# Performance work log

Measured on AMD Instinct MI355X. Metric: run time of the kernel, lower is better.

The kernel has to match this reference:

```python
import jax, jax.numpy as jnp
import numpy as np
import math

PAD_IDX = 1
BOS_IDX = 2
B, S, T = 32, 128, 64
E, H, L, V = 256, 512, 2, 32000


def _lstm_cell(gates, c):
    # torch gate order: i, f, g, o
    i, f, g, o = jnp.split(gates, 4, axis=-1)
    c_new = jax.nn.sigmoid(f) * c + jax.nn.sigmoid(i) * jnp.tanh(g)
    h_new = jax.nn.sigmoid(o) * jnp.tanh(c_new)
    return h_new, c_new


def _run_lstm_layer(x_tbi, Wih, Whh, b, h0, c0):
    def step(carry, x_t):
        h, c = carry
        h2, c2 = _lstm_cell(x_t @ Wih + h @ Whh + b, c)
        return (h2, c2), h2
    (hT, cT), ys = jax.lax.scan(step, (h0, c0), x_tbi)
    return ys, hT, cT


def setup_inputs() -> dict:
    key = jax.random.key(0)
    ks = iter(jax.random.split(key, 40))
    def w(shape, s=0.05):
        return jax.random.normal(next(ks), shape, jnp.float32) * s
    inp = {
        'src_tokens': jax.random.randint(next(ks), (B, S), 0, V, dtype=jnp.int32),
        'tgt_tokens': jax.random.randint(next(ks), (B, T), 0, V, dtype=jnp.int32),
        'src_emb': w((V, E), 0.02),
        'tgt_emb': w((V, E), 0.02),
        'enc_Wih0': w((E, 4 * H)), 'enc_Whh0': w((H, 4 * H)), 'enc_b0': jnp.zeros((4 * H,), jnp.float32),
        'enc_Wih1': w((H, 4 * H)), 'enc_Whh1': w((H, 4 * H)), 'enc_b1': jnp.zeros((4 * H,), jnp.float32),
        'dec_Wih0': w((E + H, 4 * H)), 'dec_Whh0': w((H, 4 * H)), 'dec_b0': jnp.zeros((4 * H,), jnp.float32),
        'dec_Wih1': w((H, 4 * H)), 'dec_Whh1': w((H, 4 * H)), 'dec_b1': jnp.zeros((4 * H,), jnp.float32),
        'attn_W': w((2 * H, H)), 'attn_b': jnp.zeros((H,), jnp.float32),
        'v_w': w((H,)),
        'coal_w': w((L, 1), 0.5), 'coal_b': jnp.zeros((1,), jnp.float32),
        'out_W': w((2 * H + E, V)), 'out_b': jnp.zeros((V,), jnp.float32),
    }
    return inp


def reference(src_tokens, tgt_tokens, src_emb, tgt_emb,
              enc_Wih0, enc_Whh0, enc_b0, enc_Wih1, enc_Whh1, enc_b1,
              dec_Wih0, dec_Whh0, dec_b0, dec_Wih1, dec_Whh1, dec_b1,
              attn_W, attn_b, v_w, coal_w, coal_b, out_W, out_b):
    Bq = src_tokens.shape[0]
    sqrtE_src = np.float32(math.sqrt(src_emb.shape[1]))
    sqrtE_tgt = np.float32(math.sqrt(tgt_emb.shape[1]))

    # ---- Encoder (2-layer LSTM, batch_first; dropout=0 eval) ----
    x = (src_emb[src_tokens] * sqrtE_src).transpose(1, 0, 2)  # (S,B,E)
    z = jnp.zeros((Bq, H), jnp.float32)
    ys0, hA, cA = _run_lstm_layer(x, enc_Wih0, enc_Whh0, enc_b0, z, z)
    ys1, hB, cB = _run_lstm_layer(ys0, enc_Wih1, enc_Whh1, enc_b1, z, z)
    enc_out = ys1.transpose(1, 0, 2)          # (B,S,H)
    hidden = jnp.stack([hA, hB])              # (L,B,H)
    cell = jnp.stack([cA, cB])

    mask = src_tokens != PAD_IDX              # (B,S)
    Wq, We = attn_W[:H], attn_W[H:]
    enc_proj = enc_out @ We                   # (B,S,H) loop-invariant part of attn linear

    def dec_step(carry, tok):
        h, c = carry                          # (L,B,H) each
        emb = jax.nn.relu(tgt_emb[tok] * sqrtE_tgt)          # (B,E)
        # faithful raw reshape (L,B,H) -> (B,H,L), coalesce layers
        q = jax.nn.relu(h.reshape(Bq, H, L) @ coal_w + coal_b)[..., 0]  # (B,H)
        e = jnp.tanh(enc_proj + (q @ Wq + attn_b)[:, None, :])          # (B,S,H)
        score = e @ v_w                                                 # (B,S)
        score = jnp.where(mask, score, np.float32(-1e10))
        a = jax.nn.softmax(score, axis=1)
        wctx = jnp.einsum('bs,bsh->bh', a, enc_out)                     # (B,H)
        xin = jnp.concatenate([emb, wctx], axis=-1)                     # (B,E+H)
        h0n, c0n = _lstm_cell(xin @ dec_Wih0 + h[0] @ dec_Whh0 + dec_b0, c[0])
        h1n, c1n = _lstm_cell(h0n @ dec_Wih1 + h[1] @ dec_Whh1 + dec_b1, c[1])
        logits = jnp.concatenate([h1n, wctx, emb], axis=-1) @ out_W + out_b  # (B,V)
        return (jnp.stack([h0n, h1n]), jnp.stack([c0n, c1n])), logits

    (hF, cF), outs = jax.lax.scan(dec_step, (hidden, cell), tgt_tokens[:, :-1].T)
    first = jnp.full((Bq, 1, out_b.shape[0]), np.float32(BOS_IDX))  # decoder_outputs[:,0]=BOS_IDX
    dec_outputs = jnp.concatenate([first, outs.transpose(1, 0, 2)], axis=1)  # (B,T,V)
    return dec_outputs, hF, cF
```

## Files before the change

kernel.cpp:

```cpp
#include <hip/hip_runtime.h>
#include <hip/hip_bf16.h>

typedef __bf16 bf16x8 __attribute__((ext_vector_type(8)));
typedef float f32x4 __attribute__((ext_vector_type(4)));
typedef unsigned long long u64;

#define DEV static __device__ __forceinline__

constexpr int Bq = 32, Sq = 128, Tq = 64, Eq = 256, Hq = 512, Vq = 32000;
constexpr int G4 = 2048;
constexpr int TD = 63;
constexpr int KOUT = 1280;
constexpr float SQRTE = 16.0f;

DEV float sigf(float x) { return 1.0f / (1.0f + __expf(-x)); }
DEV float tanh_fast(float x) {
    float ax = fabsf(x);
    float t = __expf(-2.f * ax);
    float r = (1.f - t) / (1.f + t);
    return x < 0.f ? -r : r;
}
DEV float tanh_c(float x) {
    float xc = fminf(fmaxf(x, -15.f), 15.f);
    float t = __expf(2.f * xc);
    return (t - 1.f) / (t + 1.f);
}

DEV u64 ldc(const u64* p) {
    return __hip_atomic_load(p, __ATOMIC_RELAXED, __HIP_MEMORY_SCOPE_AGENT);
}
DEV unsigned ldc32(const unsigned* p) {
    return __hip_atomic_load(p, __ATOMIC_RELAXED, __HIP_MEMORY_SCOPE_AGENT);
}
DEV void stc(u64* p, u64 v) {
    __hip_atomic_store(p, v, __ATOMIC_RELAXED, __HIP_MEMORY_SCOPE_AGENT);
}
DEV void stc32(unsigned* p, unsigned v) {
    __hip_atomic_store(p, v, __ATOMIC_RELAXED, __HIP_MEMORY_SCOPE_AGENT);
}
DEV unsigned short bfbits(float f) {
    __bf16 h = (__bf16)f;
    return __builtin_bit_cast(unsigned short, h);
}
DEV float bf2f(unsigned short u) {
    __bf16 h = __builtin_bit_cast(__bf16, u);
    return (float)h;
}
DEV u64 pack4bf(float a, float b, float c, float d) {
    return (u64)bfbits(a) | ((u64)bfbits(b) << 16) |
           ((u64)bfbits(c) << 32) | ((u64)bfbits(d) << 48);
}
DEV u64 pack2f(float a, float b) {
    return (u64)__float_as_uint(a) | ((u64)__float_as_uint(b) << 32);
}

DEV void gbar(unsigned* flags, int nblk, unsigned epoch) {
    __syncthreads();
    if (threadIdx.x < 64) {
        if (threadIdx.x == 0) {
            asm volatile("s_waitcnt vmcnt(0)" ::: "memory");
            stc32(flags + blockIdx.x * 32, epoch);
        }
        int lane = threadIdx.x;
        for (;;) {
            unsigned v0 = (lane < nblk) ? ldc32(flags + lane * 32) : epoch;
            unsigned v1 = (lane + 64 < nblk) ? ldc32(flags + (lane + 64) * 32) : epoch;
            if (__all((int)((v0 >= epoch) && (v1 >= epoch)))) break;
            __builtin_amdgcn_s_sleep(1);
        }
    }
    __syncthreads();
}

__global__ __launch_bounds__(256) void k_embed_src(const int* __restrict__ tok,
                                                   const float* __restrict__ emb,
                                                   __hip_bfloat16* __restrict__ x)
{
    int idx = blockIdx.x * 256 + threadIdx.x;
    int e = idx & (Eq - 1);
    int r = idx >> 8;
    int b = r & 31, t = r >> 5;
    x[idx] = __float2bfloat16(emb[(size_t)tok[b * Sq + t] * Eq + e] * SQRTE);
}

__global__ __launch_bounds__(256) void k_embed_tgt(const int* __restrict__ tok,
                                                   const float* __restrict__ emb,
                                                   __hip_bfloat16* __restrict__ embt,
                                                   __hip_bfloat16* __restrict__ Xout)
{
    int idx = blockIdx.x * 256 + threadIdx.x;
    int e = idx & (Eq - 1);
    int r = idx >> 8;
    int b = r & 31, t = r >> 5;
    float v = fmaxf(0.f, emb[(size_t)tok[b * Tq + t] * Eq + e] * SQRTE);
    embt[idx] = __float2bfloat16(v);
    Xout[(size_t)r * KOUT + 1024 + e] = __float2bfloat16(v);
}

__global__ __launch_bounds__(256) void k_transpose_bf16(const float* __restrict__ W,
                                                        __hip_bfloat16* __restrict__ Wt,
                                                        int K, int N)
{
    __shared__ float tile[32][33];
    int nb = blockIdx.x * 32, kb = blockIdx.y * 32;
    int c = threadIdx.x & 31, r4 = threadIdx.x >> 5;
    for (int i = 0; i < 32; i += 8)
        tile[r4 + i][c] = W[(size_t)(kb + r4 + i) * N + nb + c];
    __syncthreads();
    for (int i = 0; i < 32; i += 8) {
        int rr = r4 + i;
        Wt[(size_t)(nb + rr) * K + kb + c] = __float2bfloat16(tile[c][rr]);
    }
}

DEV void stage_coh(const u64* src, __bf16* As) {
    int tx = threadIdx.x;
#pragma unroll
    for (int p = 0; p < 8; ++p) {
        int c = tx + p * 256;
        int row = c >> 6, kc = c & 63;
        u64 v0 = ldc(src + c * 2);
        u64 v1 = ldc(src + c * 2 + 1);
        int kd = kc ^ (row & 7);
        *(u64*)(As + row * 512 + kd * 8) = v0;
        *(u64*)(As + row * 512 + kd * 8 + 4) = v1;
    }
}

DEV void mfma_pass(const __bf16* As, const unsigned short* BT, int colB,
                   int kg, int fr, f32x4* acc) {
    const unsigned short* bp = BT + (size_t)colB * 512 + kg * 8;
    int f7 = fr & 7;
#pragma unroll
    for (int k0 = 0; k0 < 512; k0 += 32) {
        int cidx = ((k0 >> 3) | kg) ^ f7;
        bf16x8 bfv = *(const bf16x8*)(bp + k0);
        bf16x8 af0 = *(const bf16x8*)(As + fr * 512 + cidx * 8);
        bf16x8 af1 = *(const bf16x8*)(As + (16 + fr) * 512 + cidx * 8);
        acc[0] = __builtin_amdgcn_mfma_f32_16x16x32_bf16(af0, bfv, acc[0], 0, 0, 0);
        acc[1] = __builtin_amdgcn_mfma_f32_16x16x32_bf16(af1, bfv, acc[1], 0, 0, 0);
    }
}

DEV void mfma_gates(const __bf16* As0, const __bf16* As1,
                    const __hip_bfloat16* B0T, const __hip_bfloat16* B1T,
                    int j0, float* gbuf)
{
    int tx = threadIdx.x, w = tx >> 6, lane = tx & 63;
    int fr = lane & 15, kg = lane >> 4;
    int colB = w * 512 + j0 + fr;
    f32x4 acc[2];
    acc[0] = (f32x4){0.f, 0.f, 0.f, 0.f};
    acc[1] = (f32x4){0.f, 0.f, 0.f, 0.f};
    mfma_pass(As0, (const unsigned short*)B0T, colB, kg, fr, acc);
    if (B1T) mfma_pass(As1, (const unsigned short*)B1T, colB, kg, fr, acc);
    __syncthreads();
    float* gw = gbuf + w * 512;
#pragma unroll
    for (int m = 0; m < 2; ++m)
#pragma unroll
        for (int qd = 0; qd < 4; ++qd)
            gw[(m * 16 + kg * 4 + qd) * 16 + fr] = acc[m][qd];
    __syncthreads();
}

DEV void gh_pass(const u64* hsrc, const __hip_bfloat16* WT,
                 float* slab_tile, int j0, __bf16* As0)
{
    stage_coh(hsrc, As0);
    __syncthreads();
    int tx = threadIdx.x, w = tx >> 6, lane = tx & 63;
    int fr = lane & 15, kg = lane >> 4;
    int colB = w * 512 + j0 + fr;
    f32x4 acc[2];
    acc[0] = (f32x4){0.f, 0.f, 0.f, 0.f};
    acc[1] = (f32x4){0.f, 0.f, 0.f, 0.f};
    mfma_pass(As0, (const unsigned short*)WT, colB, kg, fr, acc);
    float* outp = slab_tile + w * 512;
#pragma unroll
    for (int m = 0; m < 2; ++m)
#pragma unroll
        for (int qd = 0; qd < 4; ++qd)
            stc32((unsigned*)(outp + (m * 16 + kg * 4 + qd) * 16 + fr),
                  __float_as_uint(acc[m][qd]));
}

DEV void cell_epi(const float* gbuf, const float* gadd,
                  const __hip_bfloat16* xpart, const float* bias,
                  float* cbuf, u64* hb, u64* hf,
                  __hip_bfloat16* eb, int ebs, int j0)
{
    int tx = threadIdx.x;
    if (tx >= 128) return;
    int b = tx >> 2, jg = tx & 3;
    int jj0 = jg * 4;
    int j = j0 + jj0;
    float g[4][4];
#pragma unroll
    for (int gi = 0; gi < 4; ++gi) {
        int idx = gi * 512 + b * 16 + jj0;
        float4 gv = *(const float4*)(gbuf + idx);
        g[gi][0] = gv.x; g[gi][1] = gv.y; g[gi][2] = gv.z; g[gi][3] = gv.w;
        if (gadd) {
            u64 p0 = ldc((const u64*)gadd + (idx >> 1));
            u64 p1 = ldc((const u64*)gadd + (idx >> 1) + 1);
            g[gi][0] += __uint_as_float((unsigned)(p0 & 0xffffffffu));
            g[gi][1] += __uint_as_float((unsigned)(p0 >> 32));
            g[gi][2] += __uint_as_float((unsigned)(p1 & 0xffffffffu));
            g[gi][3] += __uint_as_float((unsigned)(p1 >> 32));
        }
        if (xpart) {
            u64 xv = *(const u64*)((const unsigned short*)xpart + b * 2048 + gi * 512 + j);
#pragma unroll
            for (int e = 0; e < 4; ++e)
                g[gi][e] += bf2f((unsigned short)(xv >> (16 * e)));
        }
        if (bias) {
            float4 bv = *(const float4*)(bias + gi * 512 + j);
            g[gi][0] += bv.x; g[gi][1] += bv.y; g[gi][2] += bv.z; g[gi][3] += bv.w;
        }
    }
    float4 cv = *(float4*)(cbuf + b * 512 + j);
    float cc[4] = {cv.x, cv.y, cv.z, cv.w};
    float hv[4];
#pragma unroll
    for (int e = 0; e < 4; ++e) {
        float cn = sigf(g[1][e]) * cc[e] + sigf(g[0][e]) * tanh_fast(g[2][e]);
        cc[e] = cn;
        hv[e] = sigf(g[3][e]) * tanh_fast(cn);
    }
    *(float4*)(cbuf + b * 512 + j) = make_float4(cc[0], cc[1], cc[2], cc[3]);
    u64 hpk = pack4bf(hv[0], hv[1], hv[2], hv[3]);
    stc(hb + ((b * 512 + j) >> 2), hpk);
    stc(hf + ((b * 512 + j) >> 1), pack2f(hv[0], hv[1]));
    stc(hf + ((b * 512 + j) >> 1) + 1, pack2f(hv[2], hv[3]));
    if (eb) *(u64*)(eb + (size_t)b * ebs + j) = hpk;
}

__global__ __launch_bounds__(256) void k_enc_persist(
    const __hip_bfloat16* __restrict__ X0b,
    const __hip_bfloat16* __restrict__ eWhh0T, const __hip_bfloat16* __restrict__ eWih1T,
    const __hip_bfloat16* __restrict__ eWhh1T, const float* __restrict__ eb1,
    __hip_bfloat16* __restrict__ h0b, __hip_bfloat16* __restrict__ h1b,
    float* __restrict__ h0f, float* __restrict__ h1f,
    float* __restrict__ c0, float* __restrict__ c1,
    __hip_bfloat16* __restrict__ ys0b,
    __hip_bfloat16* __restrict__ encb,
    unsigned* __restrict__ flags)
{
    __shared__ __align__(16) char shm[65536];
    __bf16* As0 = (__bf16*)shm;
    __bf16* As1 = (__bf16*)(shm + 32768);
    bool lay1 = blockIdx.x >= 32;
    int j0 = (blockIdx.x & 31) * 16;
    for (int t = 0; t <= 128; ++t) {
        if (!lay1) {
            if (t < 128) {
                stage_coh((const u64*)(h0b + (t & 1) * 16384), As0);
                __syncthreads();
                mfma_gates(As0, nullptr, eWhh0T, nullptr, j0, (float*)As0);
                cell_epi((float*)As0, nullptr, X0b + (size_t)t * 32 * 2048, nullptr,
                         c0, (u64*)(h0b + ((t + 1) & 1) * 16384), (u64*)h0f,
                         nullptr, 0, j0);
                if (threadIdx.x < 128) {
                    int b = threadIdx.x >> 2, jg = threadIdx.x & 3;
                    int j = j0 + jg * 4;
                    u64 hpk = ldc((const u64*)(h0b + ((t + 1) & 1) * 16384) + ((b * 512 + j) >> 2));
                    stc((u64*)(ys0b + (size_t)t * 16384 + b * 512 + j), hpk);
                }
            }
        } else {
            if (t >= 1) {
                int s = t - 1;
                stage_coh((const u64*)(ys0b + (size_t)s * 16384), As0);
                stage_coh((const u64*)(h1b + (s & 1) * 16384), As1);
                __syncthreads();
                mfma_gates(As0, As1, eWih1T, eWhh1T, j0, (float*)As0);
                cell_epi((float*)As0, nullptr, nullptr, eb1,
                         c1, (u64*)(h1b + ((s + 1) & 1) * 16384), (u64*)h1f,
                         encb + s * 512, 128 * 512, j0);
            }
        }
        gbar(flags, 64, (unsigned)(t + 1));
    }
}

__global__ __launch_bounds__(256) void k_dec_persist(
    const __hip_bfloat16* __restrict__ enc_projb, const __hip_bfloat16* __restrict__ enc_outb,
    const int* __restrict__ src_tok, const float* __restrict__ v_w,
    const float* __restrict__ attn_W, const float* __restrict__ attn_b,
    const float* __restrict__ coal_w, const float* __restrict__ coal_b,
    const __hip_bfloat16* __restrict__ dWih0wT, const __hip_bfloat16* __restrict__ dWhh0T,
    const __hip_bfloat16* __restrict__ dWih1T, const __hip_bfloat16* __restrict__ dWhh1T,
    const float* __restrict__ db1, const __hip_bfloat16* __restrict__ Xembb,
    float* __restrict__ h0fd, float* __restrict__ h1fd,
    __hip_bfloat16* __restrict__ h0bd, __hip_bfloat16* __restrict__ h1bd,
    float* __restrict__ c0d, float* __restrict__ c1d,
    __hip_bfloat16* __restrict__ wctxb,
    __hip_bfloat16* __restrict__ Xout,
    float* __restrict__ g0slab, float* __restrict__ g1slab,
    unsigned* __restrict__ flags)
{
    __shared__ __align__(16) char shm[32768];
    __shared__ float rinvs;
    __bf16* As0 = (__bf16*)shm;
    int bid = blockIdx.x, tx = threadIdx.x;
    unsigned bep = 0;

    for (int t = 0; t < TD; ++t) {
        int cur = t & 1, nxt = cur ^ 1;
        __hip_bfloat16* XoutT = Xout + (size_t)t * 32 * KOUT;

        if (bid < 32) {
            int b = bid;
            float* q   = (float*)shm;
            float* aqs = q + 512;
            float* vws = aqs + 512;
            float* ws  = vws + 512;
            const float* hrow = (b < 16) ? (h0fd + cur * 16384 + b * 1024)
                                         : (h1fd + cur * 16384 + (b - 16) * 1024);
            float cw0 = coal_w[0], cw1 = coal_w[1], cb = coal_b[0];
            for (int j = tx; j < 512; j += 256) {
                u64 pv = ldc((const u64*)hrow + j);
                float v0 = __uint_as_float((unsigned)(pv & 0xffffffffu));
                float v1 = __uint_as_float((unsigned)(pv >> 32));
                q[j] = fmaxf(0.f, v0 * cw0 + v1 * cw1 + cb);
            }
            for (int i = tx; i < 512; i += 256) vws[i] = v_w[i];
            __syncthreads();
            float a0 = attn_b[tx], a1 = attn_b[tx + 256];
#pragma unroll 8
            for (int j = 0; j < 512; ++j) {
                float qj = q[j];
                a0 += qj * attn_W[(size_t)j * 512 + tx];
                a1 += qj * attn_W[(size_t)j * 512 + tx + 256];
            }
            aqs[tx] = a0; aqs[tx + 256] = a1;
            __syncthreads();
            int s = tx >> 1, half = tx & 1;
            const unsigned short* epr = (const unsigned short*)enc_projb
                                        + ((size_t)(b * 128 + s)) * 512 + half * 256;
            float s0 = 0.f, s1 = 0.f, s2 = 0.f, s3 = 0.f;
#pragma unroll 4
            for (int ii = 0; ii < 256; ii += 8) {
                bf16x8 f8 = *(const bf16x8*)(epr + ii);
                int ib = half * 256 + ii;
                s0 += tanh_c((float)f8[0] + aqs[ib])     * vws[ib];
                s1 += tanh_c((float)f8[1] + aqs[ib + 1]) * vws[ib + 1];
                s2 += tanh_c((float)f8[2] + aqs[ib + 2]) * vws[ib + 2];
                s3 += tanh_c((float)f8[3] + aqs[ib + 3]) * vws[ib + 3];
                s0 += tanh_c((float)f8[4] + aqs[ib + 4]) * vws[ib + 4];
                s1 += tanh_c((float)f8[5] + aqs[ib + 5]) * vws[ib + 5];
                s2 += tanh_c((float)f8[6] + aqs[ib + 6]) * vws[ib + 6];
                s3 += tanh_c((float)f8[7] + aqs[ib + 7]) * vws[ib + 7];
            }
            float p = (s0 + s1) + (s2 + s3);
            p += __shfl_xor(p, 1, 64);
            if (half == 0)
                ws[s] = (src_tok[b * 128 + s] != 1) ? __expf(p) : 0.f;
            __syncthreads();
            if (tx < 64) {
                float ss = ws[tx] + ws[tx + 64];
#pragma unroll
                for (int o = 32; o > 0; o >>= 1) ss += __shfl_down(ss, o, 64);
                if (tx == 0) rinvs = 1.0f / ss;
            }
            __syncthreads();
            float rinv = rinvs;
            const unsigned short* eo = (const unsigned short*)enc_outb + (size_t)b * 65536;
            int i0 = tx * 2;
            float c0a = 0.f, c1a = 0.f;
#pragma unroll 4
            for (int s2i = 0; s2i < 128; ++s2i) {
                unsigned pk2 = *(const unsigned*)(eo + (size_t)s2i * 512 + i0);
                float wv = ws[s2i];
                c0a += wv * bf2f((unsigned short)(pk2 & 0xffffu));
                c1a += wv * bf2f((unsigned short)(pk2 >> 16));
            }
            c0a *= rinv; c1a *= rinv;
            unsigned pk = (unsigned)bfbits(c0a) | ((unsigned)bfbits(c1a) << 16);
            stc32((unsigned*)wctxb + ((b * 512 + i0) >> 1), pk);
            *((unsigned*)XoutT + (((size_t)b * KOUT + 512 + i0) >> 1)) = pk;
        } else if (bid < 64) {
            int tile = bid - 32;
            gh_pass((const u64*)(h0bd + cur * 16384), dWhh0T,
                    g0slab + tile * 2048, tile * 16, As0);
        } else {
            int tile = bid - 64;
            gh_pass((const u64*)(h1bd + cur * 16384), dWhh1T,
                    g1slab + tile * 2048, tile * 16, As0);
        }
        gbar(flags, 96, ++bep);

        if (bid < 32) {
            int j0 = bid * 16;
            stage_coh((const u64*)wctxb, As0);
            __syncthreads();
            mfma_gates(As0, nullptr, dWih0wT, nullptr, j0, (float*)As0);
            cell_epi((float*)As0, g0slab + bid * 2048,
                     Xembb + (size_t)t * 32 * 2048, nullptr,
                     c0d, (u64*)(h0bd + nxt * 16384), (u64*)(h0fd + nxt * 16384),
                     nullptr, 0, j0);
        }
        gbar(flags, 96, ++bep);

        if (bid < 32) {
            int j0 = bid * 16;
            stage_coh((const u64*)(h0bd + nxt * 16384), As0);
            __syncthreads();
            mfma_gates(As0, nullptr, dWih1T, nullptr, j0, (float*)As0);
            cell_epi((float*)As0, g1slab + bid * 2048,
                     nullptr, db1,
                     c1d, (u64*)(h1bd + nxt * 16384), (u64*)(h1fd + nxt * 16384),
                     XoutT, KOUT, j0);
        }
        gbar(flags, 96, ++bep);
    }
}

__global__ __launch_bounds__(256) void k_mfma(
    const __hip_bfloat16* __restrict__ A, const __hip_bfloat16* __restrict__ BT,
    const float* __restrict__ bias, float* __restrict__ Cf,
    __hip_bfloat16* __restrict__ Cb, int M, int N, int K)
{
    __shared__ __bf16 As[128][72];
    __shared__ __bf16 Bs[128][72];
    const unsigned short* Aw = (const unsigned short*)A;
    const unsigned short* Bw = (const unsigned short*)BT;
    int n0 = blockIdx.x * 128, m0 = blockIdx.y * 128;
    int tx = threadIdx.x;
    int w = tx >> 6, lane = tx & 63;
    int wm = (w >> 1) * 64, wn = (w & 1) * 64;
    int fr = lane & 15, kg = lane >> 4;
    f32x4 acc[4][4];
#pragma unroll
    for (int mi = 0; mi < 4; mi++)
#pragma unroll
        for (int ni = 0; ni < 4; ni++) acc[mi][ni] = (f32x4){0.f, 0.f, 0.f, 0.f};

    for (int k0 = 0; k0 < K; k0 += 64) {
        __syncthreads();
#pragma unroll
        for (int p = 0; p < 4; p++) {
            int ch = tx + p * 256;
            int r = ch >> 3, cc = (ch & 7) * 8;
            uint4 va = {0u, 0u, 0u, 0u};
            int m = m0 + r;
            if (m < M) va = *(const uint4*)(Aw + (size_t)m * K + k0 + cc);
            *(uint4*)(&As[r][cc]) = va;
            uint4 vb = *(const uint4*)(Bw + (size_t)(n0 + r) * K + k0 + cc);
            *(uint4*)(&Bs[r][cc]) = vb;
        }
        __syncthreads();
#pragma unroll
        for (int kk = 0; kk < 64; kk += 32) {
            bf16x8 af[4], bfv[4];
#pragma unroll
            for (int i = 0; i < 4; i++) {
                af[i]  = *(const bf16x8*)(&As[wm + i * 16 + fr][kk + kg * 8]);
                bfv[i] = *(const bf16x8*)(&Bs[wn + i * 16 + fr][kk + kg * 8]);
            }
#pragma unroll
            for (int mi = 0; mi < 4; mi++)
#pragma unroll
                for (int ni = 0; ni < 4; ni++)
                    acc[mi][ni] = __builtin_amdgcn_mfma_f32_16x16x32_bf16(
                        af[mi], bfv[ni], acc[mi][ni], 0, 0, 0);
        }
    }
#pragma unroll
    for (int ni = 0; ni < 4; ni++) {
        int n = n0 + wn + ni * 16 + fr;
        float bv = bias ? bias[n] : 0.f;
#pragma unroll
        for (int mi = 0; mi < 4; mi++) {
#pragma unroll
            for (int qd = 0; qd < 4; qd++) {
                int R = m0 + wm + mi * 16 + kg * 4 + qd;
                if (R < M) {
                    float v = acc[mi][ni][qd] + bv;
                    if (Cf) Cf[(size_t)R * N + n] = v;
                    else    Cb[(size_t)R * N + n] = __float2bfloat16(v);
                }
            }
        }
    }
}

__global__ __launch_bounds__(256) void k_init_dec(
    const float* __restrict__ h0e, const float* __restrict__ h1e,
    const float* __restrict__ c0e, const float* __restrict__ c1e,
    float* __restrict__ h0fd, float* __restrict__ h1fd,
    __hip_bfloat16* __restrict__ h0bd, __hip_bfloat16* __restrict__ h1bd,
    float* __restrict__ c0d, float* __restrict__ c1d)
{
    int idx = blockIdx.x * 256 + threadIdx.x;
    float a = h0e[idx], b = h1e[idx];
    h0fd[idx] = a; h1fd[idx] = b;
    h0bd[idx] = __float2bfloat16(a);
    h1bd[idx] = __float2bfloat16(b);
    c0d[idx] = c0e[idx];
    c1d[idx] = c1e[idx];
}

__global__ __launch_bounds__(256) void k_bos(float* __restrict__ out)
{
    int b = blockIdx.y;
    int i = blockIdx.x * 256 + threadIdx.x;
    out[(size_t)b * (Tq * Vq) + i] = 2.0f;
}

__global__ __launch_bounds__(256) void k_finalize(
    const float* __restrict__ h0f, const float* __restrict__ h1f,
    const float* __restrict__ c0f, const float* __restrict__ c1f,
    float* __restrict__ out)
{
    int idx = blockIdx.x * 256 + threadIdx.x;
    size_t base = (size_t)Bq * Tq * Vq;
    out[base + idx] = h0f[idx];
    out[base + 16384 + idx] = h1f[idx];
    out[base + 32768 + idx] = c0f[idx];
    out[base + 49152 + idx] = c1f[idx];
}

__global__ __launch_bounds__(256) void k_logits(
    const __hip_bfloat16* __restrict__ A, const __hip_bfloat16* __restrict__ Bt,
    const float* __restrict__ bias, float* __restrict__ out)
{
    __shared__ __bf16 As[128][72];
    __shared__ __bf16 Bs[128][72];
    const unsigned short* Aw = (const unsigned short*)A;
    const unsigned short* Bw = (const unsigned short*)Bt;
    int n0 = blockIdx.x * 128, m0 = blockIdx.y * 128;
    int tx = threadIdx.x;
    int w = tx >> 6, lane = tx & 63;
    int wm = (w >> 1) * 64, wn = (w & 1) * 64;
    int fr = lane & 15, kg = lane >> 4;
    f32x4 acc[4][4];
#pragma unroll
    for (int mi = 0; mi < 4; mi++)
#pragma unroll
        for (int ni = 0; ni < 4; ni++) acc[mi][ni] = (f32x4){0.f, 0.f, 0.f, 0.f};

    for (int k0 = 0; k0 < 1280; k0 += 64) {
        __syncthreads();
#pragma unroll
        for (int p = 0; p < 4; p++) {
            int ch = tx + p * 256;
            int r = ch >> 3, cc = (ch & 7) * 8;
            uint4 va = {0u, 0u, 0u, 0u};
            int m = m0 + r;
            if (m < 2016) va = *(const uint4*)(Aw + (size_t)m * 1280 + k0 + cc);
            *(uint4*)(&As[r][cc]) = va;
            uint4 vb = *(const uint4*)(Bw + (size_t)(n0 + r) * 1280 + k0 + cc);
            *(uint4*)(&Bs[r][cc]) = vb;
        }
        __syncthreads();
#pragma unroll
        for (int kk = 0; kk < 64; kk += 32) {
            bf16x8 af[4], bfv[4];
#pragma unroll
            for (int i = 0; i < 4; i++) {
                af[i]  = *(const bf16x8*)(&As[wm + i * 16 + fr][kk + kg * 8]);
                bfv[i] = *(const bf16x8*)(&Bs[wn + i * 16 + fr][kk + kg * 8]);
            }
#pragma unroll
            for (int mi = 0; mi < 4; mi++)
#pragma unroll
                for (int ni = 0; ni < 4; ni++)
                    acc[mi][ni] = __builtin_amdgcn_mfma_f32_16x16x32_bf16(
                        af[mi], bfv[ni], acc[mi][ni], 0, 0, 0);
        }
    }
#pragma unroll
    for (int ni = 0; ni < 4; ni++) {
        int n = n0 + wn + ni * 16 + fr;
        float bv = bias[n];
#pragma unroll
        for (int mi = 0; mi < 4; mi++) {
#pragma unroll
            for (int qd = 0; qd < 4; qd++) {
                int R = m0 + wm + mi * 16 + kg * 4 + qd;
                if (R < 2016) {
                    int bb = R & 31, ts = R >> 5;
                    out[(size_t)bb * (Tq * Vq) + (size_t)(ts + 1) * Vq + n] =
                        acc[mi][ni][qd] + bv;
                }
            }
        }
    }
}

extern "C" void kernel_launch(void* const* d_in, const int* in_sizes, int n_in,
                              void* d_out, int out_size, void* d_ws, size_t ws_size,
                              hipStream_t stream)
{
    (void)in_sizes; (void)n_in; (void)out_size; (void)ws_size;
    const int*   src_tok = (const int*)  d_in[0];
    const int*   tgt_tok = (const int*)  d_in[1];
    const float* src_emb = (const float*)d_in[2];
    const float* tgt_emb = (const float*)d_in[3];
    const float* eWih0   = (const float*)d_in[4];
    const float* eWhh0   = (const float*)d_in[5];
    const float* eb0     = (const float*)d_in[6];
    const float* eWih1   = (const float*)d_in[7];
    const float* eWhh1   = (const float*)d_in[8];
    const float* eb1     = (const float*)d_in[9];
    const float* dWih0   = (const float*)d_in[10];
    const float* dWhh0   = (const float*)d_in[11];
    const float* db0     = (const float*)d_in[12];
    const float* dWih1   = (const float*)d_in[13];
    const float* dWhh1   = (const float*)d_in[14];
    const float* db1     = (const float*)d_in[15];
    const float* attn_W  = (const float*)d_in[16];
    const float* attn_b  = (const float*)d_in[17];
    const float* v_w     = (const float*)d_in[18];
    const float* coal_w  = (const float*)d_in[19];
    const float* coal_b  = (const float*)d_in[20];
    const float* out_W   = (const float*)d_in[21];
    const float* out_b   = (const float*)d_in[22];
    float* out = (float*)d_out;

    char* ws = (char*)d_ws;
    size_t off = 0;
    auto alloc = [&](size_t bytes) -> char* {
        char* p = ws + off;
        off += (bytes + 255) & ~(size_t)255;
        return p;
    };
    typedef __hip_bfloat16 BF;
    BF* X0b     = (BF*)alloc(4096ull * 2048 * 2);
    BF* Xembb   = (BF*)alloc(2016ull * 2048 * 2);
    BF* x_srcb  = (BF*)alloc(4096ull * 256 * 2);
    BF* embtb   = (BF*)alloc(2016ull * 256 * 2);
    BF* ys0b    = (BF*)alloc(128ull * 16384 * 2);
    BF* enc_outb  = (BF*)alloc(4096ull * 512 * 2);
    BF* enc_projb = (BF*)alloc(4096ull * 512 * 2);
    BF* wctxb     = (BF*)alloc(16384ull * 2);
    BF* Xout      = (BF*)alloc(2016ull * 1280 * 2);
    BF* Wt        = (BF*)alloc(32000ull * 1280 * 2);
    BF* eWhh0T  = (BF*)alloc(2048ull * 512 * 2);
    BF* eWih1T  = (BF*)alloc(2048ull * 512 * 2);
    BF* eWhh1T  = (BF*)alloc(2048ull * 512 * 2);
    BF* dWih0wT = (BF*)alloc(2048ull * 512 * 2);
    BF* dWhh0T  = (BF*)alloc(2048ull * 512 * 2);
    BF* dWih1T  = (BF*)alloc(2048ull * 512 * 2);
    BF* dWhh1T  = (BF*)alloc(2048ull * 512 * 2);
    BF* eWih0T  = (BF*)alloc(2048ull * 256 * 2);
    BF* dWih0eT = (BF*)alloc(2048ull * 256 * 2);
    BF* WeT     = (BF*)alloc(512ull * 512 * 2);
    BF* h0b_e   = (BF*)alloc(2ull * 16384 * 2);
    BF* h1b_e   = (BF*)alloc(2ull * 16384 * 2);
    float* h0f_e = (float*)alloc(16384ull * 4);
    float* h1f_e = (float*)alloc(16384ull * 4);
    float* c0e   = (float*)alloc(16384ull * 4);
    float* c1e   = (float*)alloc(16384ull * 4);
    float* h0fd  = (float*)alloc(2ull * 16384 * 4);
    float* h1fd  = (float*)alloc(2ull * 16384 * 4);
    BF* h0bd     = (BF*)alloc(2ull * 16384 * 2);
    BF* h1bd     = (BF*)alloc(2ull * 16384 * 2);
    float* c0d   = (float*)alloc(16384ull * 4);
    float* c1d   = (float*)alloc(16384ull * 4);
    float* g0slab = (float*)alloc(32ull * 2048 * 4);
    float* g1slab = (float*)alloc(32ull * 2048 * 4);
    unsigned* encFlags = (unsigned*)alloc(64 * 32 * 4);
    unsigned* decFlags = (unsigned*)alloc(96 * 32 * 4);

    hipMemsetAsync(encFlags, 0, 64 * 32 * 4, stream);
    hipMemsetAsync(decFlags, 0, 96 * 32 * 4, stream);
    hipMemsetAsync(h0b_e, 0, 2 * 16384 * 2, stream);
    hipMemsetAsync(h1b_e, 0, 2 * 16384 * 2, stream);
    hipMemsetAsync(c0e, 0, 16384 * 4, stream);
    hipMemsetAsync(c1e, 0, 16384 * 4, stream);

    k_embed_src<<<4096, 256, 0, stream>>>(src_tok, src_emb, x_srcb);
    k_embed_tgt<<<2016, 256, 0, stream>>>(tgt_tok, tgt_emb, embtb, Xout);

    k_transpose_bf16<<<dim3(64, 16), 256, 0, stream>>>(eWhh0, eWhh0T, 512, 2048);
    k_transpose_bf16<<<dim3(64, 16), 256, 0, stream>>>(eWih1, eWih1T, 512, 2048);
    k_transpose_bf16<<<dim3(64, 16), 256, 0, stream>>>(eWhh1, eWhh1T, 512, 2048);
    k_transpose_bf16<<<dim3(64, 16), 256, 0, stream>>>(dWih0 + 256 * 2048, dWih0wT, 512, 2048);
    k_transpose_bf16<<<dim3(64, 16), 256, 0, stream>>>(dWhh0, dWhh0T, 512, 2048);
    k_transpose_bf16<<<dim3(64, 16), 256, 0, stream>>>(dWih1, dWih1T, 512, 2048);
    k_transpose_bf16<<<dim3(64, 16), 256, 0, stream>>>(dWhh1, dWhh1T, 512, 2048);
    k_transpose_bf16<<<dim3(64, 8), 256, 0, stream>>>(eWih0, eWih0T, 256, 2048);
    k_transpose_bf16<<<dim3(64, 8), 256, 0, stream>>>(dWih0, dWih0eT, 256, 2048);
    k_transpose_bf16<<<dim3(16, 16), 256, 0, stream>>>(attn_W + 512 * 512, WeT, 512, 512);
    k_transpose_bf16<<<dim3(1000, 40), 256, 0, stream>>>(out_W, Wt, 1280, 32000);

    k_mfma<<<dim3(16, 32), 256, 0, stream>>>(x_srcb, eWih0T, eb0, nullptr, X0b, 4096, 2048, 256);
    k_mfma<<<dim3(16, 16), 256, 0, stream>>>(embtb, dWih0eT, db0, nullptr, Xembb, 2016, 2048, 256);
    k_bos<<<dim3(125, 32), 256, 0, stream>>>(out);

    k_enc_persist<<<64, 256, 0, stream>>>(X0b, eWhh0T, eWih1T, eWhh1T, eb1,
                                          h0b_e, h1b_e, h0f_e, h1f_e, c0e, c1e,
                                          ys0b, enc_outb, encFlags);

    k_mfma<<<dim3(4, 32), 256, 0, stream>>>(enc_outb, WeT, nullptr, nullptr, enc_projb, 4096, 512, 512);

    k_init_dec<<<64, 256, 0, stream>>>(h0f_e, h1f_e, c0e, c1e,
                                       h0fd, h1fd, h0bd, h1bd, c0d, c1d);

    k_dec_persist<<<96, 256, 0, stream>>>(enc_projb, enc_outb, src_tok, v_w,
                                          attn_W, attn_b, coal_w, coal_b,
                                          dWih0wT, dWhh0T, dWih1T, dWhh1T,
                                          db1, Xembb,
                                          h0fd, h1fd, h0bd, h1bd, c0d, c1d,
                                          wctxb, Xout, g0slab, g1slab, decFlags);

    k_finalize<<<64, 256, 0, stream>>>(h0fd + (TD & 1) * 16384, h1fd + (TD & 1) * 16384,
                                       c0d, c1d, out);
    k_logits<<<dim3(250, 16), 256, 0, stream>>>(Xout, Wt, out_b, out);
}
```

Before: 5.788 ms.

## Replace persistent decoder kernel with per-step kernel launches instead of grid barriers

The persistent 96-block decoder kernel, which synchronised its three phases with software grid barriers, is split into three kernels (attention plus hidden-gate GEMM, layer-0 cell, layer-1 cell) launched 63 times each from the host. Kernel boundaries now provide the ordering, so coherent loads and stores are replaced with plain ones through a template flag. The grid barrier is also trimmed to poll only 64 flags, which is enough for the encoder's 64 blocks. This gives up the persistent design and adds about 189 kernel launches, each with its own launch latency, in exchange for removing the atomic barrier spins and coherent memory traffic.

```diff
diff --git a/kernel.cpp b/kernel.cpp
--- a/kernel.cpp
+++ b/kernel.cpp
@@ -54,6 +54,9 @@
     return (u64)__float_as_uint(a) | ((u64)__float_as_uint(b) << 32);
 }
 
+template<bool C> DEV u64 ld64(const u64* p) { return C ? ldc(p) : *p; }
+template<bool C> DEV void st64(u64* p, u64 v) { if (C) stc(p, v); else *p = v; }
+
 DEV void gbar(unsigned* flags, int nblk, unsigned epoch) {
     __syncthreads();
     if (threadIdx.x < 64) {
@@ -64,8 +67,7 @@
         int lane = threadIdx.x;
         for (;;) {
             unsigned v0 = (lane < nblk) ? ldc32(flags + lane * 32) : epoch;
-            unsigned v1 = (lane + 64 < nblk) ? ldc32(flags + (lane + 64) * 32) : epoch;
-            if (__all((int)((v0 >= epoch) && (v1 >= epoch)))) break;
+            if (__all((int)(v0 >= epoch))) break;
             __builtin_amdgcn_s_sleep(1);
         }
     }
@@ -113,14 +115,15 @@
     }
 }
 
-DEV void stage_coh(const u64* src, __bf16* As) {
+template<bool C>
+DEV void stage_a(const u64* src, __bf16* As) {
     int tx = threadIdx.x;
 #pragma unroll
     for (int p = 0; p < 8; ++p) {
         int c = tx + p * 256;
         int row = c >> 6, kc = c & 63;
-        u64 v0 = ldc(src + c * 2);
-        u64 v1 = ldc(src + c * 2 + 1);
+        u64 v0 = ld64<C>(src + c * 2);
+        u64 v1 = ld64<C>(src + c * 2 + 1);
         int kd = kc ^ (row & 7);
         *(u64*)(As + row * 512 + kd * 8) = v0;
         *(u64*)(As + row * 512 + kd * 8 + 4) = v1;
@@ -164,27 +167,7 @@
     __syncthreads();
 }
 
-DEV void gh_pass(const u64* hsrc, const __hip_bfloat16* WT,
-                 float* slab_tile, int j0, __bf16* As0)
-{
-    stage_coh(hsrc, As0);
-    __syncthreads();
-    int tx = threadIdx.x, w = tx >> 6, lane = tx & 63;
-    int fr = lane & 15, kg = lane >> 4;
-    int colB = w * 512 + j0 + fr;
-    f32x4 acc[2];
-    acc[0] = (f32x4){0.f, 0.f, 0.f, 0.f};
-    acc[1] = (f32x4){0.f, 0.f, 0.f, 0.f};
-    mfma_pass(As0, (const unsigned short*)WT, colB, kg, fr, acc);
-    float* outp = slab_tile + w * 512;
-#pragma unroll
-    for (int m = 0; m < 2; ++m)
-#pragma unroll
-        for (int qd = 0; qd < 4; ++qd)
-            stc32((unsigned*)(outp + (m * 16 + kg * 4 + qd) * 16 + fr),
-                  __float_as_uint(acc[m][qd]));
-}
-
+template<bool C>
 DEV void cell_epi(const float* gbuf, const float* gadd,
                   const __hip_bfloat16* xpart, const float* bias,
                   float* cbuf, u64* hb, u64* hf,
@@ -202,12 +185,8 @@
         float4 gv = *(const float4*)(gbuf + idx);
         g[gi][0] = gv.x; g[gi][1] = gv.y; g[gi][2] = gv.z; g[gi][3] = gv.w;
         if (gadd) {
-            u64 p0 = ldc((const u64*)gadd + (idx >> 1));
-            u64 p1 = ldc((const u64*)gadd + (idx >> 1) + 1);
-            g[gi][0] += __uint_as_float((unsigned)(p0 & 0xffffffffu));
-            g[gi][1] += __uint_as_float((unsigned)(p0 >> 32));
-            g[gi][2] += __uint_as_float((unsigned)(p1 & 0xffffffffu));
-            g[gi][3] += __uint_as_float((unsigned)(p1 >> 32));
+            float4 ga = *(const float4*)(gadd + idx);
+            g[gi][0] += ga.x; g[gi][1] += ga.y; g[gi][2] += ga.z; g[gi][3] += ga.w;
         }
         if (xpart) {
             u64 xv = *(const u64*)((const unsigned short*)xpart + b * 2048 + gi * 512 + j);
@@ -231,10 +210,10 @@
     }
     *(float4*)(cbuf + b * 512 + j) = make_float4(cc[0], cc[1], cc[2], cc[3]);
     u64 hpk = pack4bf(hv[0], hv[1], hv[2], hv[3]);
-    stc(hb + ((b * 512 + j) >> 2), hpk);
-    stc(hf + ((b * 512 + j) >> 1), pack2f(hv[0], hv[1]));
-    stc(hf + ((b * 512 + j) >> 1) + 1, pack2f(hv[2], hv[3]));
-    if (eb) *(u64*)(eb + (size_t)b * ebs + j) = hpk;
+    st64<C>(hb + ((b * 512 + j) >> 2), hpk);
+    st64<C>(hf + ((b * 512 + j) >> 1), pack2f(hv[0], hv[1]));
+    st64<C>(hf + ((b * 512 + j) >> 1) + 1, pack2f(hv[2], hv[3]));
+    if (eb) st64<C>((u64*)(eb + (size_t)b * ebs + j), hpk);
 }
 
 __global__ __launch_bounds__(256) void k_enc_persist(
@@ -256,12 +235,12 @@
     for (int t = 0; t <= 128; ++t) {
         if (!lay1) {
             if (t < 128) {
-                stage_coh((const u64*)(h0b + (t & 1) * 16384), As0);
+                stage_a<true>((const u64*)(h0b + (t & 1) * 16384), As0);
                 __syncthreads();
                 mfma_gates(As0, nullptr, eWhh0T, nullptr, j0, (float*)As0);
-                cell_epi((float*)As0, nullptr, X0b + (size_t)t * 32 * 2048, nullptr,
-                         c0, (u64*)(h0b + ((t + 1) & 1) * 16384), (u64*)h0f,
-                         nullptr, 0, j0);
+                cell_epi<true>((float*)As0, nullptr, X0b + (size_t)t * 32 * 2048, nullptr,
+                               c0, (u64*)(h0b + ((t + 1) & 1) * 16384), (u64*)h0f,
+                               nullptr, 0, j0);
                 if (threadIdx.x < 128) {
                     int b = threadIdx.x >> 2, jg = threadIdx.x & 3;
                     int j = j0 + jg * 4;
@@ -272,150 +251,155 @@
         } else {
             if (t >= 1) {
                 int s = t - 1;
-                stage_coh((const u64*)(ys0b + (size_t)s * 16384), As0);
-                stage_coh((const u64*)(h1b + (s & 1) * 16384), As1);
+                stage_a<true>((const u64*)(ys0b + (size_t)s * 16384), As0);
+                stage_a<true>((const u64*)(h1b + (s & 1) * 16384), As1);
                 __syncthreads();
                 mfma_gates(As0, As1, eWih1T, eWhh1T, j0, (float*)As0);
-                cell_epi((float*)As0, nullptr, nullptr, eb1,
-                         c1, (u64*)(h1b + ((s + 1) & 1) * 16384), (u64*)h1f,
-                         encb + s * 512, 128 * 512, j0);
+                cell_epi<true>((float*)As0, nullptr, nullptr, eb1,
+                               c1, (u64*)(h1b + ((s + 1) & 1) * 16384), (u64*)h1f,
+                               encb + s * 512, 128 * 512, j0);
             }
         }
         gbar(flags, 64, (unsigned)(t + 1));
     }
 }
 
-__global__ __launch_bounds__(256) void k_dec_persist(
+__global__ __launch_bounds__(256) void k_dattn(
     const __hip_bfloat16* __restrict__ enc_projb, const __hip_bfloat16* __restrict__ enc_outb,
     const int* __restrict__ src_tok, const float* __restrict__ v_w,
     const float* __restrict__ attn_W, const float* __restrict__ attn_b,
     const float* __restrict__ coal_w, const float* __restrict__ coal_b,
-    const __hip_bfloat16* __restrict__ dWih0wT, const __hip_bfloat16* __restrict__ dWhh0T,
-    const __hip_bfloat16* __restrict__ dWih1T, const __hip_bfloat16* __restrict__ dWhh1T,
-    const float* __restrict__ db1, const __hip_bfloat16* __restrict__ Xembb,
-    float* __restrict__ h0fd, float* __restrict__ h1fd,
-    __hip_bfloat16* __restrict__ h0bd, __hip_bfloat16* __restrict__ h1bd,
-    float* __restrict__ c0d, float* __restrict__ c1d,
-    __hip_bfloat16* __restrict__ wctxb,
-    __hip_bfloat16* __restrict__ Xout,
-    float* __restrict__ g0slab, float* __restrict__ g1slab,
-    unsigned* __restrict__ flags)
+    const __hip_bfloat16* __restrict__ dWhh0T, const __hip_bfloat16* __restrict__ dWhh1T,
+    const float* __restrict__ h0fc, const float* __restrict__ h1fc,
+    const __hip_bfloat16* __restrict__ h0bc, const __hip_bfloat16* __restrict__ h1bc,
+    __hip_bfloat16* __restrict__ wctxb, __hip_bfloat16* __restrict__ XoutT,
+    float* __restrict__ g0slab, float* __restrict__ g1slab)
 {
     __shared__ __align__(16) char shm[32768];
     __shared__ float rinvs;
     __bf16* As0 = (__bf16*)shm;
     int bid = blockIdx.x, tx = threadIdx.x;
-    unsigned bep = 0;
-
-    for (int t = 0; t < TD; ++t) {
-        int cur = t & 1, nxt = cur ^ 1;
-        __hip_bfloat16* XoutT = Xout + (size_t)t * 32 * KOUT;
-
-        if (bid < 32) {
-            int b = bid;
-            float* q   = (float*)shm;
-            float* aqs = q + 512;
-            float* vws = aqs + 512;
-            float* ws  = vws + 512;
-            const float* hrow = (b < 16) ? (h0fd + cur * 16384 + b * 1024)
-                                         : (h1fd + cur * 16384 + (b - 16) * 1024);
-            float cw0 = coal_w[0], cw1 = coal_w[1], cb = coal_b[0];
-            for (int j = tx; j < 512; j += 256) {
-                u64 pv = ldc((const u64*)hrow + j);
-                float v0 = __uint_as_float((unsigned)(pv & 0xffffffffu));
-                float v1 = __uint_as_float((unsigned)(pv >> 32));
-                q[j] = fmaxf(0.f, v0 * cw0 + v1 * cw1 + cb);
-            }
-            for (int i = tx; i < 512; i += 256) vws[i] = v_w[i];
-            __syncthreads();
-            float a0 = attn_b[tx], a1 = attn_b[tx + 256];
+
+    if (bid < 32) {
+        int b = bid;
+        float* q   = (float*)shm;
+        float* aqs = q + 512;
+        float* vws = aqs + 512;
+        float* ws  = vws + 512;
+        const float* hrow = (b < 16) ? (h0fc + b * 1024) : (h1fc + (b - 16) * 1024);
+        float cw0 = coal_w[0], cw1 = coal_w[1], cb = coal_b[0];
+        for (int j = tx; j < 512; j += 256) {
+            float2 pv = *(const float2*)(hrow + 2 * j);
+            q[j] = fmaxf(0.f, pv.x * cw0 + pv.y * cw1 + cb);
+        }
+        for (int i = tx; i < 512; i += 256) vws[i] = v_w[i];
+        __syncthreads();
+        float a0 = attn_b[tx], a1 = attn_b[tx + 256];
 #pragma unroll 8
-            for (int j = 0; j < 512; ++j) {
-                float qj = q[j];
-                a0 += qj * attn_W[(size_t)j * 512 + tx];
-                a1 += qj * attn_W[(size_t)j * 512 + tx + 256];
-            }
-            aqs[tx] = a0; aqs[tx + 256] = a1;
-            __syncthreads();
-            int s = tx >> 1, half = tx & 1;
-            const unsigned short* epr = (const unsigned short*)enc_projb
-                                        + ((size_t)(b * 128 + s)) * 512 + half * 256;
-            float s0 = 0.f, s1 = 0.f, s2 = 0.f, s3 = 0.f;
+        for (int j = 0; j < 512; ++j) {
+            float qj = q[j];
+            a0 += qj * attn_W[(size_t)j * 512 + tx];
+            a1 += qj * attn_W[(size_t)j * 512 + tx + 256];
+        }
+        aqs[tx] = a0; aqs[tx + 256] = a1;
+        __syncthreads();
+        int s = tx >> 1, half = tx & 1;
+        const unsigned short* epr = (const unsigned short*)enc_projb
+                                    + ((size_t)(b * 128 + s)) * 512 + half * 256;
+        float s0 = 0.f, s1 = 0.f, s2 = 0.f, s3 = 0.f;
 #pragma unroll 4
-            for (int ii = 0; ii < 256; ii += 8) {
-                bf16x8 f8 = *(const bf16x8*)(epr + ii);
-                int ib = half * 256 + ii;
-                s0 += tanh_c((float)f8[0] + aqs[ib])     * vws[ib];
-                s1 += tanh_c((float)f8[1] + aqs[ib + 1]) * vws[ib + 1];
-                s2 += tanh_c((float)f8[2] + aqs[ib + 2]) * vws[ib + 2];
-                s3 += tanh_c((float)f8[3] + aqs[ib + 3]) * vws[ib + 3];
-                s0 += tanh_c((float)f8[4] + aqs[ib + 4]) * vws[ib + 4];
-                s1 += tanh_c((float)f8[5] + aqs[ib + 5]) * vws[ib + 5];
-                s2 += tanh_c((float)f8[6] + aqs[ib + 6]) * vws[ib + 6];
-                s3 += tanh_c((float)f8[7] + aqs[ib + 7]) * vws[ib + 7];
-            }
-            float p = (s0 + s1) + (s2 + s3);
-            p += __shfl_xor(p, 1, 64);
-            if (half == 0)
-                ws[s] = (src_tok[b * 128 + s] != 1) ? __expf(p) : 0.f;
-            __syncthreads();
-            if (tx < 64) {
-                float ss = ws[tx] + ws[tx + 64];
-#pragma unroll
-                for (int o = 32; o > 0; o >>= 1) ss += __shfl_down(ss, o, 64);
-                if (tx == 0) rinvs = 1.0f / ss;
-            }
-            __syncthreads();
-            float rinv = rinvs;
-            const unsigned short* eo = (const unsigned short*)enc_outb + (size_t)b * 65536;
-            int i0 = tx * 2;
-            float c0a = 0.f, c1a = 0.f;
+        for (int ii = 0; ii < 256; ii += 8) {
+            bf16x8 f8 = *(const bf16x8*)(epr + ii);
+            int ib = half * 256 + ii;
+            s0 += tanh_c((float)f8[0] + aqs[ib])     * vws[ib];
+            s1 += tanh_c((float)f8[1] + aqs[ib + 1]) * vws[ib + 1];
+            s2 += tanh_c((float)f8[2] + aqs[ib + 2]) * vws[ib + 2];
+            s3 += tanh_c((float)f8[3] + aqs[ib + 3]) * vws[ib + 3];
+            s0 += tanh_c((float)f8[4] + aqs[ib + 4]) * vws[ib + 4];
+            s1 += tanh_c((float)f8[5] + aqs[ib + 5]) * vws[ib + 5];
+            s2 += tanh_c((float)f8[6] + aqs[ib + 6]) * vws[ib + 6];
+            s3 += tanh_c((float)f8[7] + aqs[ib + 7]) * vws[ib + 7];
+        }
+        float p = (s0 + s1) + (s2 + s3);
+        p += __shfl_xor(p, 1, 64);
+        if (half == 0)
+            ws[s] = (src_tok[b * 128 + s] != 1) ? __expf(p) : 0.f;
+        __syncthreads();
+        if (tx < 64) {
+            float ss = ws[tx] + ws[tx + 64];
+#pragma unroll
+            for (int o = 32; o > 0; o >>= 1) ss += __shfl_down(ss, o, 64);
+            if (tx == 0) rinvs = 1.0f / ss;
+        }
+        __syncthreads();
+        float rinv = rinvs;
+        const unsigned short* eo = (const unsigned short*)enc_outb + (size_t)b * 65536;
+        int i0 = tx * 2;
+        float c0a = 0.f, c1a = 0.f;
 #pragma unroll 4
-            for (int s2i = 0; s2i < 128; ++s2i) {
-                unsigned pk2 = *(const unsigned*)(eo + (size_t)s2i * 512 + i0);
-                float wv = ws[s2i];
-                c0a += wv * bf2f((unsigned short)(pk2 & 0xffffu));
-                c1a += wv * bf2f((unsigned short)(pk2 >> 16));
-            }
-            c0a *= rinv; c1a *= rinv;
-            unsigned pk = (unsigned)bfbits(c0a) | ((unsigned)bfbits(c1a) << 16);
-            stc32((unsigned*)wctxb + ((b * 512 + i0) >> 1), pk);
-            *((unsigned*)XoutT + (((size_t)b * KOUT + 512 + i0) >> 1)) = pk;
-        } else if (bid < 64) {
-            int tile = bid - 32;
-            gh_pass((const u64*)(h0bd + cur * 16384), dWhh0T,
-                    g0slab + tile * 2048, tile * 16, As0);
-        } else {
-            int tile = bid - 64;
-            gh_pass((const u64*)(h1bd + cur * 16384), dWhh1T,
-                    g1slab + tile * 2048, tile * 16, As0);
-        }
-        gbar(flags, 96, ++bep);
-
-        if (bid < 32) {
-            int j0 = bid * 16;
-            stage_coh((const u64*)wctxb, As0);
-            __syncthreads();
-            mfma_gates(As0, nullptr, dWih0wT, nullptr, j0, (float*)As0);
-            cell_epi((float*)As0, g0slab + bid * 2048,
-                     Xembb + (size_t)t * 32 * 2048, nullptr,
-                     c0d, (u64*)(h0bd + nxt * 16384), (u64*)(h0fd + nxt * 16384),
-                     nullptr, 0, j0);
-        }
-        gbar(flags, 96, ++bep);
-
-        if (bid < 32) {
-            int j0 = bid * 16;
-            stage_coh((const u64*)(h0bd + nxt * 16384), As0);
-            __syncthreads();
-            mfma_gates(As0, nullptr, dWih1T, nullptr, j0, (float*)As0);
-            cell_epi((float*)As0, g1slab + bid * 2048,
-                     nullptr, db1,
-                     c1d, (u64*)(h1bd + nxt * 16384), (u64*)(h1fd + nxt * 16384),
-                     XoutT, KOUT, j0);
-        }
-        gbar(flags, 96, ++bep);
-    }
+        for (int s2i = 0; s2i < 128; ++s2i) {
+            unsigned pk2 = *(const unsigned*)(eo + (size_t)s2i * 512 + i0);
+            float wv = ws[s2i];
+            c0a += wv * bf2f((unsigned short)(pk2 & 0xffffu));
+            c1a += wv * bf2f((unsigned short)(pk2 >> 16));
+        }
+        c0a *= rinv; c1a *= rinv;
+        unsigned pk = (unsigned)bfbits(c0a) | ((unsigned)bfbits(c1a) << 16);
+        *((unsigned*)wctxb + ((b * 512 + i0) >> 1)) = pk;
+        *((unsigned*)XoutT + (((size_t)b * KOUT + 512 + i0) >> 1)) = pk;
+    } else {
+        int tile = (bid < 64) ? bid - 32 : bid - 64;
+        const __hip_bfloat16* hsrc = (bid < 64) ? h0bc : h1bc;
+        const __hip_bfloat16* WT = (bid < 64) ? dWhh0T : dWhh1T;
+        float* slab = ((bid < 64) ? g0slab : g1slab) + tile * 2048;
+        int j0 = tile * 16;
+        stage_a<false>((const u64*)hsrc, As0);
+        __syncthreads();
+        int w = tx >> 6, lane = tx & 63;
+        int fr = lane & 15, kg = lane >> 4;
+        int colB = w * 512 + j0 + fr;
+        f32x4 acc[2];
+        acc[0] = (f32x4){0.f, 0.f, 0.f, 0.f};
+        acc[1] = (f32x4){0.f, 0.f, 0.f, 0.f};
+        mfma_pass(As0, (const unsigned short*)WT, colB, kg, fr, acc);
+        float* outp = slab + w * 512;
+#pragma unroll
+        for (int m = 0; m < 2; ++m)
+#pragma unroll
+            for (int qd = 0; qd < 4; ++qd)
+                outp[(m * 16 + kg * 4 + qd) * 16 + fr] = acc[m][qd];
+    }
+}
+
+__global__ __launch_bounds__(256) void k_dcell0(
+    const __hip_bfloat16* __restrict__ wctxb, const __hip_bfloat16* __restrict__ Wih0wT,
+    const __hip_bfloat16* __restrict__ xpart, const float* __restrict__ g0slab,
+    float* __restrict__ c0d, __hip_bfloat16* __restrict__ hb_nxt, float* __restrict__ hf_nxt)
+{
+    __shared__ __align__(16) char shm[32768];
+    __bf16* As0 = (__bf16*)shm;
+    int j0 = blockIdx.x * 16;
+    stage_a<false>((const u64*)wctxb, As0);
+    __syncthreads();
+    mfma_gates(As0, nullptr, Wih0wT, nullptr, j0, (float*)As0);
+    cell_epi<false>((float*)As0, g0slab + blockIdx.x * 2048, xpart, nullptr,
+                    c0d, (u64*)hb_nxt, (u64*)hf_nxt, nullptr, 0, j0);
+}
+
+__global__ __launch_bounds__(256) void k_dcell1(
+    const __hip_bfloat16* __restrict__ h0b_nxt, const __hip_bfloat16* __restrict__ Wih1T,
+    const float* __restrict__ db1, const float* __restrict__ g1slab,
+    float* __restrict__ c1d, __hip_bfloat16* __restrict__ hb_nxt, float* __restrict__ hf_nxt,
+    __hip_bfloat16* __restrict__ XoutT)
+{
+    __shared__ __align__(16) char shm[32768];
+    __bf16* As0 = (__bf16*)shm;
+    int j0 = blockIdx.x * 16;
+    stage_a<false>((const u64*)h0b_nxt, As0);
+    __syncthreads();
+    mfma_gates(As0, nullptr, Wih1T, nullptr, j0, (float*)As0);
+    cell_epi<false>((float*)As0, g1slab + blockIdx.x * 2048, nullptr, db1,
+                    c1d, (u64*)hb_nxt, (u64*)hf_nxt, XoutT, KOUT, j0);
 }
 
 __global__ __launch_bounds__(256) void k_mfma(
@@ -664,10 +648,8 @@
     float* g0slab = (float*)alloc(32ull * 2048 * 4);
     float* g1slab = (float*)alloc(32ull * 2048 * 4);
     unsigned* encFlags = (unsigned*)alloc(64 * 32 * 4);
-    unsigned* decFlags = (unsigned*)alloc(96 * 32 * 4);
 
     hipMemsetAsync(encFlags, 0, 64 * 32 * 4, stream);
-    hipMemsetAsync(decFlags, 0, 96 * 32 * 4, stream);
     hipMemsetAsync(h0b_e, 0, 2 * 16384 * 2, stream);
     hipMemsetAsync(h1b_e, 0, 2 * 16384 * 2, stream);
     hipMemsetAsync(c0e, 0, 16384 * 4, stream);
@@ -701,12 +683,22 @@
     k_init_dec<<<64, 256, 0, stream>>>(h0f_e, h1f_e, c0e, c1e,
                                        h0fd, h1fd, h0bd, h1bd, c0d, c1d);
 
-    k_dec_persist<<<96, 256, 0, stream>>>(enc_projb, enc_outb, src_tok, v_w,
-                                          attn_W, attn_b, coal_w, coal_b,
-                                          dWih0wT, dWhh0T, dWih1T, dWhh1T,
-                                          db1, Xembb,
-                                          h0fd, h1fd, h0bd, h1bd, c0d, c1d,
-                                          wctxb, Xout, g0slab, g1slab, decFlags);
+    for (int t = 0; t < TD; ++t) {
+        int cur = t & 1, nxt = cur ^ 1;
+        BF* XoutT = Xout + (size_t)t * 32 * KOUT;
+        k_dattn<<<96, 256, 0, stream>>>(enc_projb, enc_outb, src_tok, v_w,
+                                        attn_W, attn_b, coal_w, coal_b,
+                                        dWhh0T, dWhh1T,
+                                        h0fd + cur * 16384, h1fd + cur * 16384,
+                                        h0bd + cur * 16384, h1bd + cur * 16384,
+                                        wctxb, XoutT, g0slab, g1slab);
+        k_dcell0<<<32, 256, 0, stream>>>(wctxb, dWih0wT,
+                                         Xembb + (size_t)t * 32 * 2048, g0slab,
+                                         c0d, h0bd + nxt * 16384, h0fd + nxt * 16384);
+        k_dcell1<<<32, 256, 0, stream>>>(h0bd + nxt * 16384, dWih1T, db1, g1slab,
+                                         c1d, h1bd + nxt * 16384, h1fd + nxt * 16384,
+                                         XoutT);
+    }
 
     k_finalize<<<64, 256, 0, stream>>>(h0fd + (TD & 1) * 16384, h1fd + (TD & 1) * 16384,
                                        c0d, c1d, out);
```

Result: faster. 5.480 ms (-5.3%).
